# Performance work log

Measured on AMD Instinct MI355X. Metric: run time of the kernel, lower is better.

## Reference

```python
import jax, jax.numpy as jnp
import numpy as np

EPS = 1e-12
ATTEND_SCALE = 8.0

def _l2norm(t, axis=-1):
    n = jnp.sqrt(jnp.sum(t * t, axis=axis, keepdims=True))
    return t / jnp.maximum(n, EPS)

def setup_inputs() -> dict:
    key = jax.random.key(0)
    k1, k2, k3, k4 = jax.random.split(key, 4)
    b, n, dim = 4, 8192, 1024
    heads, dim_head = 16, 64
    dim_inner = heads * dim_head
    x = jax.random.normal(k1, (b, n, dim), dtype=jnp.float32)
    gamma = jnp.ones((dim,), dtype=jnp.float32)  # RMSNorm gamma
    # torch Linear(dim, 3*dim_inner, bias=False): store as [dim, 3*dim_inner] for x @ W
    w_qkv = jax.random.normal(k2, (dim, 3 * dim_inner), dtype=jnp.float32) * (dim ** -0.5)
    temperature = jnp.zeros((heads, 1, 1), dtype=jnp.float32)
    w_out = jax.random.normal(k3, (dim_inner, dim), dtype=jnp.float32) * (dim_inner ** -0.5)
    return {"x": x, "gamma": gamma, "w_qkv": w_qkv, "temperature": temperature, "w_out": w_out}

def reference(x, gamma, w_qkv, temperature, w_out):
    b, n, dim = x.shape
    heads = temperature.shape[0]
    dim_head = w_qkv.shape[1] // (3 * heads)
    # RMSNorm: F.normalize(x, dim=-1) * sqrt(dim) * gamma
    xn = _l2norm(x) * (dim ** 0.5) * gamma
    qkv = xn @ w_qkv  # [b, n, 3*h*d]
    qkv = qkv.reshape(b, n, 3, heads, dim_head).transpose(2, 0, 3, 4, 1)  # [3, b, h, d, n]
    q, k, v = qkv[0], qkv[1], qkv[2]
    orig_v = v
    # l2-normalize q, k over the sequence axis (last dim of [b,h,d,n])
    q = _l2norm(q) * jnp.exp(temperature)  # temperature [h,1,1] broadcasts
    k = _l2norm(k)
    # attention over the feature axis: sim [b, h, d, d]
    sim = jnp.einsum('bhdn,bhen->bhde', q, k) * ATTEND_SCALE
    attn = jax.nn.softmax(sim, axis=-1)
    out = jnp.einsum('bhde,bhen->bhdn', attn, v)  # [b, h, d, n]
    out = out.transpose(0, 3, 1, 2).reshape(b, n, heads * dim_head) @ w_out  # [b, n, dim]
    return out, orig_v
```

## Files before the change

### kernel.cpp

```cpp
#include <hip/hip_runtime.h>
#include <hip/hip_bf16.h>

#define DEVI __device__ __forceinline__

using bf16x8 = __attribute__((ext_vector_type(8))) __bf16;
using f32x4  = __attribute__((ext_vector_type(4))) float;
using u16x8  = __attribute__((ext_vector_type(8))) unsigned short;

DEVI unsigned short f2bf(float f) {
  unsigned int u = __float_as_uint(f);
  u = (u + 0x7FFFu + ((u >> 16) & 1u)) >> 16;
  return (unsigned short)u;
}
DEVI float bf2f(unsigned short s) { return __uint_as_float(((unsigned int)s) << 16); }

DEVI void gld_lds16(const unsigned short* g, unsigned short* l) {
  __builtin_amdgcn_global_load_lds(
      (const __attribute__((address_space(1))) void*)g,
      (__attribute__((address_space(3))) void*)l, 16, 0, 0);
}

__global__ __launch_bounds__(256) void transpose_cast_kernel(const float* __restrict__ in,
                                                             unsigned short* __restrict__ out,
                                                             int R, int C) {
  __shared__ float tile[32][33];
  const int c0 = blockIdx.x * 32, r0 = blockIdx.y * 32;
  const int tx = threadIdx.x & 31, ty = threadIdx.x >> 5;
  for (int rr = ty; rr < 32; rr += 8)
    tile[rr][tx] = in[(size_t)(r0 + rr) * C + c0 + tx];
  __syncthreads();
  for (int cc = ty; cc < 32; cc += 8)
    out[(size_t)(c0 + cc) * R + r0 + tx] = f2bf(tile[tx][cc]);
}

__global__ __launch_bounds__(256) void castv_kernel(const float* __restrict__ w_qkv,
                                                    unsigned short* __restrict__ Wv_nt) {
  const int i = blockIdx.x * 256 + threadIdx.x;
  const int k = i >> 8, he4 = (i & 255) * 4;
  const float4 v = *(const float4*)&w_qkv[(size_t)k * 3072 + 2048 + he4];
  ushort4 o;
  o.x = f2bf(v.x); o.y = f2bf(v.y); o.z = f2bf(v.z); o.w = f2bf(v.w);
  *(ushort4*)&Wv_nt[(size_t)k * 1024 + he4] = o;
}

__global__ __launch_bounds__(256) void transpose_bf16x4_kernel(const unsigned short* __restrict__ in,
                                                               unsigned short* __restrict__ out) {
  __shared__ unsigned short tile[64][68];
  const int r0 = blockIdx.x * 64;
  const int c0 = blockIdx.y * 64;
  const int t = threadIdx.x;
  const int tr = t >> 4, tc4 = (t & 15) * 4;
#pragma unroll
  for (int p = 0; p < 4; ++p) {
    const int rr = p * 16 + tr;
    *(ushort4*)&tile[rr][tc4] = *(const ushort4*)&in[(size_t)(r0 + rr) * 1024 + c0 + tc4];
  }
  __syncthreads();
#pragma unroll
  for (int p = 0; p < 4; ++p) {
    const int cc = p * 16 + tr;
    ushort4 o;
    o.x = tile[tc4 + 0][cc];
    o.y = tile[tc4 + 1][cc];
    o.z = tile[tc4 + 2][cc];
    o.w = tile[tc4 + 3][cc];
    *(ushort4*)&out[(size_t)(c0 + cc) * 32768 + r0 + tc4] = o;
  }
}

__global__ __launch_bounds__(256) void rmsnorm_kernel(const float* __restrict__ x,
                                                      const float* __restrict__ gamma,
                                                      unsigned short* __restrict__ xn) {
  __shared__ float wsum[4];
  const int row = blockIdx.x;
  const int t = threadIdx.x;
  const float4 v = *(const float4*)&x[(size_t)row * 1024 + t * 4];
  float s = v.x * v.x + v.y * v.y + v.z * v.z + v.w * v.w;
  for (int off = 32; off; off >>= 1) s += __shfl_down(s, off);
  if ((t & 63) == 0) wsum[t >> 6] = s;
  __syncthreads();
  const float tot = wsum[0] + wsum[1] + wsum[2] + wsum[3];
  const float scale = 32.0f / fmaxf(sqrtf(tot), 1e-12f);
  const float4 g = *(const float4*)&gamma[t * 4];
  ushort4 o;
  o.x = f2bf(v.x * scale * g.x);
  o.y = f2bf(v.y * scale * g.y);
  o.z = f2bf(v.z * scale * g.z);
  o.w = f2bf(v.w * scale * g.w);
  *(ushort4*)&xn[(size_t)row * 1024 + t * 4] = o;
}

DEVI void stage256(const unsigned short* __restrict__ gA,
                   const unsigned short* __restrict__ gB,
                   unsigned short* lA, unsigned short* lB,
                   int k0, int w, int lane, size_t gstride) {
  const int dr = lane >> 3;
  const int ks = (lane & 7) ^ dr;
  const size_t lo = (size_t)dr * gstride + k0 + ks * 8;
#pragma unroll
  for (int i = 0; i < 4; ++i) {
    const int oct = w * 4 + i;
    gld_lds16(gA + (size_t)oct * 8 * gstride + lo, lA + oct * 512 + lane * 8);
    gld_lds16(gB + (size_t)oct * 8 * gstride + lo, lB + oct * 512 + lane * 8);
  }
}

DEVI void compute256(const unsigned short* __restrict__ lA,
                     const unsigned short* __restrict__ lB,
                     int wm, int wn, int lane, f32x4 (&acc)[8][4]) {
  const int r = lane & 15, kg = lane >> 4;
  const int r7 = r & 7;
#pragma unroll
  for (int ksl = 0; ksl < 2; ++ksl) {
    const int sA = (((ksl << 2) + kg) ^ r7) * 8;
    bf16x8 af[8], bfr[4];
#pragma unroll
    for (int m = 0; m < 8; ++m)
      af[m] = *(const bf16x8*)&lA[(wm * 128 + m * 16 + r) * 64 + sA];
#pragma unroll
    for (int n = 0; n < 4; ++n)
      bfr[n] = *(const bf16x8*)&lB[(wn * 64 + n * 16 + r) * 64 + sA];
#pragma unroll
    for (int m = 0; m < 8; ++m)
#pragma unroll
      for (int n = 0; n < 4; ++n)
        acc[m][n] = __builtin_amdgcn_mfma_f32_16x16x32_bf16(af[m], bfr[n], acc[m][n], 0, 0, 0);
  }
}

#define VOUT_BAR()  __builtin_amdgcn_sched_barrier(0); __builtin_amdgcn_s_barrier(); \
                    __builtin_amdgcn_sched_barrier(0)
#define VOUT_W8()   asm volatile("s_waitcnt vmcnt(8)" ::: "memory")
#define VOUT_W0()   asm volatile("s_waitcnt vmcnt(0)" ::: "memory")

__global__ __launch_bounds__(512, 2) void gemm_gram256_kernel(
    const unsigned short* __restrict__ xnT, unsigned short* __restrict__ Gp) {
  if (blockIdx.x > blockIdx.y) return;
  __shared__ __align__(16) unsigned short Al[2][16384];
  __shared__ __align__(16) unsigned short Bl[2][16384];
  const int tid = threadIdx.x;
  const int lane = tid & 63;
  const int w = tid >> 6;
  const int wm = w >> 2, wn = w & 3;
  const int z = blockIdx.z;
  const size_t koff = (size_t)(z >> 2) * 8192 + (size_t)(z & 3) * 2048;
  const unsigned short* gA = xnT + (size_t)blockIdx.y * 256 * 32768 + koff;
  const unsigned short* gB = xnT + (size_t)blockIdx.x * 256 * 32768 + koff;

  f32x4 acc[8][4] = {};
  stage256(gA, gB, Al[0], Bl[0], 0, w, lane, 32768);
#pragma unroll 1
  for (int tt = 0; tt < 15; ++tt) {
    stage256(gA, gB, Al[1], Bl[1], (tt * 2 + 1) * 64, w, lane, 32768);
    VOUT_W8(); VOUT_BAR();
    __builtin_amdgcn_s_setprio(1);
    compute256(Al[0], Bl[0], wm, wn, lane, acc);
    __builtin_amdgcn_s_setprio(0);
    VOUT_BAR();
    stage256(gA, gB, Al[0], Bl[0], (tt * 2 + 2) * 64, w, lane, 32768);
    VOUT_W8(); VOUT_BAR();
    __builtin_amdgcn_s_setprio(1);
    compute256(Al[1], Bl[1], wm, wn, lane, acc);
    __builtin_amdgcn_s_setprio(0);
    VOUT_BAR();
  }
  stage256(gA, gB, Al[1], Bl[1], 31 * 64, w, lane, 32768);
  VOUT_W8(); VOUT_BAR();
  __builtin_amdgcn_s_setprio(1);
  compute256(Al[0], Bl[0], wm, wn, lane, acc);
  __builtin_amdgcn_s_setprio(0);
  VOUT_BAR();
  VOUT_W0(); VOUT_BAR();
  __builtin_amdgcn_s_setprio(1);
  compute256(Al[1], Bl[1], wm, wn, lane, acc);
  __builtin_amdgcn_s_setprio(0);

  unsigned short* C = Gp + ((size_t)z << 20);
  const int rr = (lane >> 4) * 4;
  const int cc = lane & 15;
  const size_t grow0 = (size_t)blockIdx.y * 256 + wm * 128;
  const int gc0 = blockIdx.x * 256 + wn * 64;
#pragma unroll
  for (int m = 0; m < 8; ++m)
#pragma unroll
    for (int n = 0; n < 4; ++n)
#pragma unroll
      for (int j = 0; j < 4; ++j)
        C[(grow0 + m * 16 + rr + j) * 1024 + gc0 + n * 16 + cc] = f2bf(acc[m][n][j]);
}

__global__ __launch_bounds__(256) void greduce_kernel(const unsigned short* __restrict__ Gp,
                                                      unsigned short* __restrict__ G) {
  const int tj = blockIdx.x, ti = blockIdx.y, b = blockIdx.z;
  if ((tj >> 2) > (ti >> 2)) return;
  __shared__ float lds[64][65];
  const int t = threadIdx.x;
  const int r = t >> 2, c0 = (t & 3) * 16;
  const size_t idx = (size_t)(ti * 64 + r) * 1024 + tj * 64 + c0;
  float v[16];
#pragma unroll
  for (int j = 0; j < 16; ++j) v[j] = 0.f;
  for (int s = 0; s < 4; ++s) {
    const unsigned short* p = Gp + ((size_t)(b * 4 + s) << 20) + idx;
#pragma unroll
    for (int j = 0; j < 16; ++j) v[j] += bf2f(p[j]);
  }
  unsigned short* Gb = G + ((size_t)b << 20);
  __attribute__((aligned(16))) unsigned short buf[16];
#pragma unroll
  for (int j = 0; j < 16; ++j) buf[j] = f2bf(v[j]);
  { int4* dst = (int4*)&Gb[idx]; const int4* src = (const int4*)buf; dst[0] = src[0]; dst[1] = src[1]; }
  if ((ti >> 2) != (tj >> 2)) {
#pragma unroll
    for (int j = 0; j < 16; ++j) lds[r][c0 + j] = v[j];
    __syncthreads();
    const int x = t >> 2, y0 = (t & 3) * 16;
#pragma unroll
    for (int j = 0; j < 16; ++j) buf[j] = f2bf(lds[y0 + j][x]);
    int4* dst = (int4*)&Gb[(size_t)(tj * 64 + x) * 1024 + ti * 64 + y0];
    const int4* src = (const int4*)buf;
    dst[0] = src[0]; dst[1] = src[1];
  }
}

__global__ __launch_bounds__(256) void gemm_bt_batch_bf16(const unsigned short* __restrict__ A,
                                                          const unsigned short* __restrict__ Bt,
                                                          unsigned short* __restrict__ C,
                                                          int N, int K,
                                                          long long aStr, long long bStr, long long cStr) {
  __shared__ __align__(16) unsigned short Al[4096];
  __shared__ __align__(16) unsigned short Bl[4096];
  A += (size_t)blockIdx.z * aStr; Bt += (size_t)blockIdx.z * bStr; C += (size_t)blockIdx.z * cStr;
  const int tid = threadIdx.x;
  const int lane = tid & 63, wid = tid >> 6;
  const int wr = wid >> 1, wc = wid & 1;
  const int r = lane & 15, kg = lane >> 4;
  const int rw0 = tid >> 2, q0 = (tid & 3) * 8;
  const size_t row0 = (size_t)blockIdx.y * 128, col0 = (size_t)blockIdx.x * 128;
  f32x4 acc[4][4] = {};
  for (int k0 = 0; k0 < K; k0 += 32) {
    __syncthreads();
    gld_lds16(&A[(row0 + rw0) * K + k0 + q0], &Al[tid * 8]);
    gld_lds16(&A[(row0 + rw0 + 64) * K + k0 + q0], &Al[2048 + tid * 8]);
    gld_lds16(&Bt[(col0 + rw0) * K + k0 + q0], &Bl[tid * 8]);
    gld_lds16(&Bt[(col0 + rw0 + 64) * K + k0 + q0], &Bl[2048 + tid * 8]);
    __syncthreads();
    bf16x8 af[4], bfr[4];
#pragma unroll
    for (int m = 0; m < 4; ++m) af[m] = *(const bf16x8*)&Al[(wr * 64 + m * 16 + r) * 32 + kg * 8];
#pragma unroll
    for (int n = 0; n < 4; ++n) bfr[n] = *(const bf16x8*)&Bl[(wc * 64 + n * 16 + r) * 32 + kg * 8];
#pragma unroll
    for (int m = 0; m < 4; ++m)
#pragma unroll
      for (int n = 0; n < 4; ++n)
        acc[m][n] = __builtin_amdgcn_mfma_f32_16x16x32_bf16(af[m], bfr[n], acc[m][n], 0, 0, 0);
  }
  const int rbase = wr * 64 + (lane >> 4) * 4;
  const int cbase = wc * 64 + (lane & 15);
#pragma unroll
  for (int m = 0; m < 4; ++m)
#pragma unroll
    for (int n = 0; n < 4; ++n)
#pragma unroll
      for (int j = 0; j < 4; ++j)
        C[(row0 + rbase + m * 16 + j) * N + col0 + cbase + n * 16] = f2bf(acc[m][n][j]);
}

__global__ __launch_bounds__(512, 2) void gemm_vout256_kernel(
    const unsigned short* __restrict__ A,
    const unsigned short* __restrict__ BtV,
    const unsigned short* __restrict__ WfoldT,
    float* __restrict__ origv,
    float* __restrict__ outp) {
  __shared__ __align__(16) unsigned short Al[2][16384];
  __shared__ __align__(16) unsigned short Bl[2][16384];
  const int tid = threadIdx.x;
  const int lane = tid & 63;
  const int w = tid >> 6;
  const int wm = w >> 2, wn = w & 3;
  const int cb = blockIdx.x & 7;
  const int rb = blockIdx.x >> 3;
  const int b = rb >> 5;
  const unsigned short* gA = A + (size_t)rb * 256 * 1024;
  const unsigned short* gB = (cb < 4)
      ? BtV + (size_t)cb * 256 * 1024
      : WfoldT + ((size_t)b << 20) + (size_t)(cb - 4) * 256 * 1024;

  f32x4 acc[8][4] = {};
  stage256(gA, gB, Al[0], Bl[0], 0, w, lane, 1024);
#pragma unroll 1
  for (int tt = 0; tt < 7; ++tt) {
    stage256(gA, gB, Al[1], Bl[1], (tt * 2 + 1) * 64, w, lane, 1024);
    VOUT_W8(); VOUT_BAR();
    __builtin_amdgcn_s_setprio(1);
    compute256(Al[0], Bl[0], wm, wn, lane, acc);
    __builtin_amdgcn_s_setprio(0);
    VOUT_BAR();
    stage256(gA, gB, Al[0], Bl[0], (tt * 2 + 2) * 64, w, lane, 1024);
    VOUT_W8(); VOUT_BAR();
    __builtin_amdgcn_s_setprio(1);
    compute256(Al[1], Bl[1], wm, wn, lane, acc);
    __builtin_amdgcn_s_setprio(0);
    VOUT_BAR();
  }
  stage256(gA, gB, Al[1], Bl[1], 15 * 64, w, lane, 1024);
  VOUT_W8(); VOUT_BAR();
  __builtin_amdgcn_s_setprio(1);
  compute256(Al[0], Bl[0], wm, wn, lane, acc);
  __builtin_amdgcn_s_setprio(0);
  VOUT_BAR();
  VOUT_W0(); VOUT_BAR();
  __builtin_amdgcn_s_setprio(1);
  compute256(Al[1], Bl[1], wm, wn, lane, acc);
  __builtin_amdgcn_s_setprio(0);

  const int rr = (lane >> 4) * 4;
  const int cc = lane & 15;
  if (cb < 4) {
    const int nbase = (rb & 31) * 256 + wm * 128;
#pragma unroll
    for (int m = 0; m < 8; ++m)
#pragma unroll
      for (int n = 0; n < 4; ++n) {
        const int hd = cb * 256 + wn * 64 + n * 16 + cc;
        const float4 o4 = make_float4(acc[m][n][0], acc[m][n][1], acc[m][n][2], acc[m][n][3]);
        *(float4*)&origv[((size_t)b * 1024 + hd) * 8192 + nbase + m * 16 + rr] = o4;
      }
  } else {
    const size_t grow0 = (size_t)rb * 256 + wm * 128;
    const int gc0 = (cb - 4) * 256 + wn * 64;
#pragma unroll
    for (int m = 0; m < 8; ++m)
#pragma unroll
      for (int n = 0; n < 4; ++n)
#pragma unroll
        for (int j = 0; j < 4; ++j)
          outp[(grow0 + m * 16 + rr + j) * 1024 + gc0 + n * 16 + cc] = acc[m][n][j];
  }
}

__global__ __launch_bounds__(256) void norms_kernel(const unsigned short* __restrict__ UTt,
                                                    const unsigned short* __restrict__ wqkvT,
                                                    float* __restrict__ qkn2) {
  const int t = threadIdx.x;
  const int rloc = t >> 4, lane16 = t & 15;
  const int row = blockIdx.x * 16 + rloc;
  const int b = row >> 11, r2 = row & 2047;
  const unsigned short* pa = UTt + ((size_t)b << 21) + (size_t)r2 * 1024 + lane16 * 64;
  const unsigned short* pb = wqkvT + (size_t)r2 * 1024 + lane16 * 64;
  float s = 0.f;
  for (int i = 0; i < 64; i += 8) {
    const u16x8 va = *(const u16x8*)&pa[i];
    const u16x8 vb = *(const u16x8*)&pb[i];
#pragma unroll
    for (int j = 0; j < 8; ++j) s += bf2f(va[j]) * bf2f(vb[j]);
  }
  for (int off = 8; off; off >>= 1) s += __shfl_down(s, off, 16);
  if (lane16 == 0) qkn2[row] = s;
}

__global__ __launch_bounds__(256) void sim_softmax_kernel(const unsigned short* __restrict__ wqkvT,
                                                          const unsigned short* __restrict__ UTt,
                                                          const float* __restrict__ qkn2,
                                                          const float* __restrict__ temperature,
                                                          float* __restrict__ attn) {
  __shared__ __align__(16) unsigned short Aql[64 * 128];
  __shared__ __align__(16) unsigned short Bkl[64 * 128];
  __shared__ float qknl[2][64];
  const int bh = blockIdx.x;
  const int b = bh >> 4, h = bh & 15;
  const int t = threadIdx.x;
  const int lane = t & 63, w = t >> 6;
  const unsigned short* UTtb = UTt + ((size_t)b << 21);
  if (t < 128) {
    const int sel = t >> 6, dd = t & 63;
    qknl[sel][dd] = fmaxf(sqrtf(qkn2[b * 2048 + sel * 1024 + h * 64 + dd]), 1e-12f);
  }
  const unsigned short* AqG = UTtb + (size_t)(h * 64) * 1024;
  const unsigned short* BkG = wqkvT + (size_t)(1024 + h * 64) * 1024;
  const int r = lane & 15, kg = lane >> 4;
  const int srow = t >> 4, scol = (t & 15) * 8;
  f32x4 acc[4] = {};
  for (int k0 = 0; k0 < 1024; k0 += 128) {
    __syncthreads();
#pragma unroll
    for (int c = 0; c < 4; ++c) {
      gld_lds16(&AqG[(size_t)(c * 16 + srow) * 1024 + k0 + scol], &Aql[c * 2048 + t * 8]);
      gld_lds16(&BkG[(size_t)(c * 16 + srow) * 1024 + k0 + scol], &Bkl[c * 2048 + t * 8]);
    }
    __syncthreads();
#pragma unroll
    for (int kk = 0; kk < 128; kk += 32) {
      const bf16x8 af = *(const bf16x8*)&Aql[(w * 16 + r) * 128 + kk + kg * 8];
#pragma unroll
      for (int n = 0; n < 4; ++n) {
        const bf16x8 bfr = *(const bf16x8*)&Bkl[(n * 16 + r) * 128 + kk + kg * 8];
        acc[n] = __builtin_amdgcn_mfma_f32_16x16x32_bf16(af, bfr, acc[n], 0, 0, 0);
      }
    }
  }
  const float sc = 8.f * __expf(temperature[h]);
  const int colq = lane & 15, rq = lane >> 4;
#pragma unroll
  for (int j = 0; j < 4; ++j) {
    const int d = w * 16 + rq * 4 + j;
    const float qd = qknl[0][d];
    float sv[4];
#pragma unroll
    for (int n = 0; n < 4; ++n) sv[n] = acc[n][j] * sc / (qd * qknl[1][n * 16 + colq]);
    float mj = fmaxf(fmaxf(sv[0], sv[1]), fmaxf(sv[2], sv[3]));
    for (int msk = 1; msk < 16; msk <<= 1) mj = fmaxf(mj, __shfl_xor(mj, msk));
    float p[4], sum = 0.f;
#pragma unroll
    for (int n = 0; n < 4; ++n) { p[n] = __expf(sv[n] - mj); sum += p[n]; }
    for (int msk = 1; msk < 16; msk <<= 1) sum += __shfl_xor(sum, msk);
    const float inv = 1.f / sum;
#pragma unroll
    for (int n = 0; n < 4; ++n)
      attn[(size_t)bh * 4096 + d * 64 + n * 16 + colq] = p[n] * inv;
  }
}

__global__ __launch_bounds__(256) void w2t_kernel(const float* __restrict__ attn,
                                                  const float* __restrict__ w_out,
                                                  unsigned short* __restrict__ W2T) {
  __shared__ float al[64][64];
  __shared__ float wl[64][64];
  const int bh = blockIdx.y;
  const int b = bh >> 4, h = bh & 15;
  const int c0 = blockIdx.x * 256;
  const int t = threadIdx.x, e = t & 63, g = t >> 6;
  const int dr = t >> 2, q4 = (t & 3) * 16;
#pragma unroll
  for (int j = 0; j < 16; j += 4)
    *(float4*)&al[dr][q4 + j] = *(const float4*)&attn[(size_t)bh * 4096 + dr * 64 + q4 + j];
  for (int cbk = 0; cbk < 4; ++cbk) {
    __syncthreads();
#pragma unroll
    for (int j = 0; j < 16; j += 4)
      *(float4*)&wl[dr][q4 + j] = *(const float4*)&w_out[(size_t)(h * 64 + dr) * 1024 + c0 + cbk * 64 + q4 + j];
    __syncthreads();
#pragma unroll
    for (int i = 0; i < 16; ++i) {
      const int cc = g * 16 + i;
      float s = 0.f;
#pragma unroll 8
      for (int d = 0; d < 64; ++d) s += al[d][e] * wl[d][cc];
      W2T[((size_t)b << 20) + (size_t)(c0 + cbk * 64 + cc) * 1024 + h * 64 + e] = f2bf(s);
    }
  }
}

extern "C" void kernel_launch(void* const* d_in, const int* in_sizes, int n_in,
                              void* d_out, int out_size, void* d_ws, size_t ws_size,
                              hipStream_t stream) {
  const float* x     = (const float*)d_in[0];
  const float* gamma = (const float*)d_in[1];
  const float* w_qkv = (const float*)d_in[2];
  const float* temp  = (const float*)d_in[3];
  const float* w_out = (const float*)d_in[4];
  char* ws = (char*)d_ws;
  unsigned short* wqkvT  = (unsigned short*)(ws);
  unsigned short* Wv_nt  = (unsigned short*)(ws + 6291456);
  unsigned short* xn     = (unsigned short*)(ws + 8388608);
  unsigned short* xnT    = (unsigned short*)(ws + 75497472);
  unsigned short* Gp     = (unsigned short*)(ws + 142606336);
  unsigned short* G      = (unsigned short*)(ws + 176160768);
  unsigned short* UTt    = (unsigned short*)(ws + 184549376);
  float* qkn2            = (float*)(ws + 201326592);
  float* attn            = (float*)(ws + 201359360);
  unsigned short* W2T    = (unsigned short*)(ws + 202407936);
  unsigned short* WfoldT = (unsigned short*)(ws + 210796544);
  float* outp  = (float*)d_out;
  float* origv = outp + (size_t)33554432;

  transpose_cast_kernel<<<dim3(96, 32), 256, 0, stream>>>(w_qkv, wqkvT, 1024, 3072);
  castv_kernel<<<1024, 256, 0, stream>>>(w_qkv, Wv_nt);
  rmsnorm_kernel<<<32768, 256, 0, stream>>>(x, gamma, xn);
  transpose_bf16x4_kernel<<<dim3(512, 16), 256, 0, stream>>>(xn, xnT);
  gemm_gram256_kernel<<<dim3(4, 4, 16), 512, 0, stream>>>(xnT, Gp);
  greduce_kernel<<<dim3(16, 16, 4), 256, 0, stream>>>(Gp, G);
  gemm_bt_batch_bf16<<<dim3(8, 16, 4), 256, 0, stream>>>(wqkvT, G, UTt, 1024, 1024,
                                                         0LL, 1LL << 20, 1LL << 21);
  norms_kernel<<<512, 256, 0, stream>>>(UTt, wqkvT, qkn2);
  sim_softmax_kernel<<<64, 256, 0, stream>>>(wqkvT, UTt, qkn2, temp, attn);
  w2t_kernel<<<dim3(4, 64), 256, 0, stream>>>(attn, w_out, W2T);
  gemm_bt_batch_bf16<<<dim3(8, 8, 4), 256, 0, stream>>>(W2T, Wv_nt, WfoldT, 1024, 1024,
                                                        1LL << 20, 0LL, 1LL << 20);
  gemm_vout256_kernel<<<1024, 512, 0, stream>>>(xn, wqkvT + (size_t)2048 * 1024, WfoldT,
                                                origv, outp);
}
```

Before: 471.1 us.

## Restructure vout GEMM into quadrant-wise half-tile staging with finer interleaving

Rewrites the 256x256 GEMM main loop so each K-step is split into four 128x128 quadrant sub-computations, and each quadrant overlaps one half-tile async load into the other buffer. Waits become vmcnt-granular per half-tile instead of a full-tile wait. Warp tiling changes to 2x4 of 64x32 per quadrant, with register fragments reused across quadrants in a ping-pong order. The aim is to hide global-to-LDS latency better. The cost is more barriers per K-step.

```diff
diff --git a/kernel.cpp b/kernel.cpp
--- a/kernel.cpp
+++ b/kernel.cpp
@@ -267,18 +267,69 @@
         C[(row0 + rbase + m * 16 + j) * N + col0 + cbase + n * 16] = f2bf(acc[m][n][j]);
 }
 
+DEVI void stage_half(const unsigned short* __restrict__ g, unsigned short* l,
+                     int k0, int tid, size_t gstride) {
+  const int r6 = tid >> 3;
+  const int ks = (tid & 7) ^ (r6 & 7);
+  const size_t lo = (size_t)r6 * gstride + k0 + ks * 8;
+  gld_lds16(g + lo, l + tid * 8);
+  gld_lds16(g + (size_t)64 * gstride + lo, l + 4096 + tid * 8);
+}
+
+DEVI void read_a8(const unsigned short* __restrict__ lA, int Mh, int w, int lane,
+                  bf16x8 (&af)[8]) {
+  const int r = lane & 15, kg = lane >> 4, r7 = r & 7;
+  const int rowb = Mh * 128 + (w & 1) * 64;
+#pragma unroll
+  for (int ksl = 0; ksl < 2; ++ksl) {
+    const int sA = (((ksl << 2) + kg) ^ r7) * 8;
+#pragma unroll
+    for (int m = 0; m < 4; ++m)
+      af[ksl * 4 + m] = *(const bf16x8*)&lA[(rowb + m * 16 + r) * 64 + sA];
+  }
+}
+
+DEVI void read_b4(const unsigned short* __restrict__ lB, int Nh, int w, int lane,
+                  bf16x8 (&bfr)[4]) {
+  const int r = lane & 15, kg = lane >> 4, r7 = r & 7;
+  const int rowb = Nh * 128 + (w >> 1) * 32;
+#pragma unroll
+  for (int ksl = 0; ksl < 2; ++ksl) {
+    const int sA = (((ksl << 2) + kg) ^ r7) * 8;
+#pragma unroll
+    for (int n = 0; n < 2; ++n)
+      bfr[ksl * 2 + n] = *(const bf16x8*)&lB[(rowb + n * 16 + r) * 64 + sA];
+  }
+}
+
+DEVI void mfma16(const bf16x8 (&af)[8], const bf16x8 (&bfr)[4], f32x4 (&accq)[4][2]) {
+  __builtin_amdgcn_s_setprio(1);
+#pragma unroll
+  for (int ksl = 0; ksl < 2; ++ksl)
+#pragma unroll
+    for (int m = 0; m < 4; ++m)
+#pragma unroll
+      for (int n = 0; n < 2; ++n)
+        accq[m][n] = __builtin_amdgcn_mfma_f32_16x16x32_bf16(af[ksl * 4 + m], bfr[ksl * 2 + n],
+                                                             accq[m][n], 0, 0, 0);
+  __builtin_amdgcn_s_setprio(0);
+}
+
+#define VW6() asm volatile("s_waitcnt vmcnt(6)" ::: "memory")
+#define VW4() asm volatile("s_waitcnt vmcnt(4)" ::: "memory")
+#define VW2() asm volatile("s_waitcnt vmcnt(2)" ::: "memory")
+
 __global__ __launch_bounds__(512, 2) void gemm_vout256_kernel(
     const unsigned short* __restrict__ A,
     const unsigned short* __restrict__ BtV,
     const unsigned short* __restrict__ WfoldT,
     float* __restrict__ origv,
     float* __restrict__ outp) {
-  __shared__ __align__(16) unsigned short Al[2][16384];
-  __shared__ __align__(16) unsigned short Bl[2][16384];
+  __shared__ __align__(16) unsigned short lA[2][16384];
+  __shared__ __align__(16) unsigned short lB[2][16384];
   const int tid = threadIdx.x;
   const int lane = tid & 63;
   const int w = tid >> 6;
-  const int wm = w >> 2, wn = w & 3;
   const int cb = blockIdx.x & 7;
   const int rb = blockIdx.x >> 3;
   const int b = rb >> 5;
@@ -286,57 +337,82 @@
   const unsigned short* gB = (cb < 4)
       ? BtV + (size_t)cb * 256 * 1024
       : WfoldT + ((size_t)b << 20) + (size_t)(cb - 4) * 256 * 1024;
-
-  f32x4 acc[8][4] = {};
-  stage256(gA, gB, Al[0], Bl[0], 0, w, lane, 1024);
+  const unsigned short* gA1 = gA + (size_t)128 * 1024;
+  const unsigned short* gB1 = gB + (size_t)128 * 1024;
+
+  f32x4 acc[4][4][2] = {};
+  bf16x8 af[8], bfr[4];
+
+  stage_half(gA,  lA[0],        0, tid, 1024);
+  stage_half(gB,  lB[0],        0, tid, 1024);
+  stage_half(gB1, lB[0] + 8192, 0, tid, 1024);
+  stage_half(gA1, lA[0] + 8192, 0, tid, 1024);
+
 #pragma unroll 1
-  for (int tt = 0; tt < 7; ++tt) {
-    stage256(gA, gB, Al[1], Bl[1], (tt * 2 + 1) * 64, w, lane, 1024);
-    VOUT_W8(); VOUT_BAR();
-    __builtin_amdgcn_s_setprio(1);
-    compute256(Al[0], Bl[0], wm, wn, lane, acc);
-    __builtin_amdgcn_s_setprio(0);
-    VOUT_BAR();
-    stage256(gA, gB, Al[0], Bl[0], (tt * 2 + 2) * 64, w, lane, 1024);
-    VOUT_W8(); VOUT_BAR();
-    __builtin_amdgcn_s_setprio(1);
-    compute256(Al[1], Bl[1], wm, wn, lane, acc);
-    __builtin_amdgcn_s_setprio(0);
-    VOUT_BAR();
-  }
-  stage256(gA, gB, Al[1], Bl[1], 15 * 64, w, lane, 1024);
-  VOUT_W8(); VOUT_BAR();
-  __builtin_amdgcn_s_setprio(1);
-  compute256(Al[0], Bl[0], wm, wn, lane, acc);
-  __builtin_amdgcn_s_setprio(0);
-  VOUT_BAR();
-  VOUT_W0(); VOUT_BAR();
-  __builtin_amdgcn_s_setprio(1);
-  compute256(Al[1], Bl[1], wm, wn, lane, acc);
-  __builtin_amdgcn_s_setprio(0);
+  for (int t = 0; t < 16; ++t) {
+    const unsigned short* cA = lA[t & 1];
+    const unsigned short* cB = lB[t & 1];
+    unsigned short* nA = lA[(t + 1) & 1];
+    unsigned short* nB = lB[(t + 1) & 1];
+    const int k1 = (t + 1) * 64;
+    const bool more = (t < 15);
+    if (more) stage_half(gA, nA, k1, tid, 1024);
+    if (more) { VW6(); } else { VW4(); }
+    VOUT_BAR();
+    read_a8(cA, 0, w, lane, af);
+    read_b4(cB, 0, w, lane, bfr);
+    mfma16(af, bfr, acc[0]);
+    VOUT_BAR();
+    if (more) stage_half(gB, nB, k1, tid, 1024);
+    if (more) { VW6(); } else { VW2(); }
+    VOUT_BAR();
+    read_b4(cB, 1, w, lane, bfr);
+    mfma16(af, bfr, acc[1]);
+    VOUT_BAR();
+    if (more) stage_half(gB1, nB + 8192, k1, tid, 1024);
+    if (more) { VW6(); } else { VOUT_W0(); }
+    VOUT_BAR();
+    read_a8(cA, 1, w, lane, af);
+    mfma16(af, bfr, acc[2]);
+    VOUT_BAR();
+    if (more) stage_half(gA1, nA + 8192, k1, tid, 1024);
+    if (more) { VW6(); }
+    VOUT_BAR();
+    read_b4(cB, 0, w, lane, bfr);
+    mfma16(af, bfr, acc[3]);
+    VOUT_BAR();
+  }
 
   const int rr = (lane >> 4) * 4;
   const int cc = lane & 15;
-  if (cb < 4) {
-    const int nbase = (rb & 31) * 256 + wm * 128;
-#pragma unroll
-    for (int m = 0; m < 8; ++m)
-#pragma unroll
-      for (int n = 0; n < 4; ++n) {
-        const int hd = cb * 256 + wn * 64 + n * 16 + cc;
-        const float4 o4 = make_float4(acc[m][n][0], acc[m][n][1], acc[m][n][2], acc[m][n][3]);
-        *(float4*)&origv[((size_t)b * 1024 + hd) * 8192 + nbase + m * 16 + rr] = o4;
-      }
-  } else {
-    const size_t grow0 = (size_t)rb * 256 + wm * 128;
-    const int gc0 = (cb - 4) * 256 + wn * 64;
-#pragma unroll
-    for (int m = 0; m < 8; ++m)
-#pragma unroll
-      for (int n = 0; n < 4; ++n)
-#pragma unroll
-        for (int j = 0; j < 4; ++j)
-          outp[(grow0 + m * 16 + rr + j) * 1024 + gc0 + n * 16 + cc] = acc[m][n][j];
+  const int mrow0 = (w & 1) * 64;
+  const int ncol0 = (w >> 1) * 32;
+#pragma unroll
+  for (int q = 0; q < 4; ++q) {
+    const int Mh = (q == 2 || q == 3);
+    const int Nh = (q == 1 || q == 2);
+    if (cb < 4) {
+      const int nbase = (rb & 31) * 256 + Mh * 128 + mrow0;
+#pragma unroll
+      for (int m = 0; m < 4; ++m)
+#pragma unroll
+        for (int n = 0; n < 2; ++n) {
+          const int hd = cb * 256 + Nh * 128 + ncol0 + n * 16 + cc;
+          const float4 o4 = make_float4(acc[q][m][n][0], acc[q][m][n][1],
+                                        acc[q][m][n][2], acc[q][m][n][3]);
+          *(float4*)&origv[((size_t)b * 1024 + hd) * 8192 + nbase + m * 16 + rr] = o4;
+        }
+    } else {
+      const size_t grow0 = (size_t)rb * 256 + Mh * 128 + mrow0;
+      const int gc0 = (cb - 4) * 256 + Nh * 128 + ncol0;
+#pragma unroll
+      for (int m = 0; m < 4; ++m)
+#pragma unroll
+        for (int n = 0; n < 2; ++n)
+#pragma unroll
+          for (int j = 0; j < 4; ++j)
+            outp[(grow0 + m * 16 + rr + j) * 1024 + gc0 + n * 16 + cc] = acc[q][m][n][j];
+    }
   }
 }
 
```

Result: slower. 504.7 us (+7.1%).
